# Optimization experiments

Measured on AMD Instinct MI355X. Metric: run time of the kernel, lower is better.

Reference implementation:

```python
import jax, jax.numpy as jnp
import numpy as np
import math

EPS = 1e-07
ITERATIONS = 3
FINAL_LAMBDA = 0.01

B, H, W, K, CIN, COUT, P = 8, 12, 12, 3, 16, 32, 16


def setup_inputs() -> dict:
    key = jax.random.key(0)
    k1, k2, k3, k4 = jax.random.split(key, 4)
    V = jax.random.normal(k1, (B, H, W, K, K, CIN, COUT, P), dtype=jnp.float32)
    a = jax.random.uniform(k2, (B, H, W, K, K, CIN, 1), dtype=jnp.float32)
    Beta_u = jax.random.normal(k3, (1, 1, 1, 1, 1, 1, COUT, 1), dtype=jnp.float32)
    Beta_a = jax.random.normal(k4, (1, 1, 1, 1, 1, 1, COUT), dtype=jnp.float32)
    R = jnp.full((B, H, W, K, K, CIN, COUT), 1.0 / COUT, dtype=jnp.float32)
    outSize = (B, H, W, COUT, P)
    return {"V": V, "a": a, "Beta_u": Beta_u, "Beta_a": Beta_a, "R": R, "outSize": outSize}


def _l2_normalize(x, axis):
    n = jnp.sqrt(jnp.sum(x * x, axis=axis, keepdims=True))
    return x / jnp.maximum(n, 1e-12)  # matches F.normalize default eps


def reference(V, a, Beta_u, Beta_a, R, outSize):
    mathpilog = jnp.log(jnp.asarray(2.0 * math.pi, dtype=jnp.float32))
    mu = sigma_sqr = a_out = None
    for i in range(ITERATIONS):
        Lam = FINAL_LAMBDA * (1.0 - 0.95 ** (i + 1))
        Rw = (R * a)[..., None]                                  # [B,h,w,K,K,Cin,Cout,1]
        mu_denom = jnp.sum(Rw, axis=(3, 4, 5), keepdims=True)    # [B,h,w,1,1,1,Cout,1]
        mu = jnp.sum(Rw * V, axis=(3, 4, 5), keepdims=True) / (mu_denom + EPS)  # [B,h,w,1,1,1,Cout,P]
        V_mu_sqr = (V - mu) ** 2                                 # [B,h,w,K,K,Cin,Cout,P]
        sigma_sqr = jnp.sum(Rw * V_mu_sqr, axis=(3, 4, 5), keepdims=True) / (mu_denom + EPS)
        cost_h = (Beta_u + 0.5 * jnp.log(sigma_sqr)) * mu_denom  # [B,h,w,1,1,1,Cout,P]
        x = Lam * (Beta_a - jnp.sum(cost_h, axis=7))             # [B,h,w,1,1,1,Cout]
        a_out = jax.nn.sigmoid(_l2_normalize(x, axis=6))
        log_p1 = -0.5 * jnp.sum(mathpilog + jnp.log(sigma_sqr), axis=7) + EPS
        log_p2 = -jnp.sum(V_mu_sqr / (2.0 * sigma_sqr + EPS), axis=7)  # [B,h,w,K,K,Cin,Cout]
        R = jax.nn.softmax(jnp.log(a_out) + log_p1 + log_p2, axis=6)
    mu_out = jnp.squeeze(mu).reshape(outSize)
    sigma_out = jnp.squeeze(sigma_sqr).reshape(outSize)
    return mu_out, jnp.squeeze(a_out), sigma_out
```

## Files before the change

### kernel.cpp

```cpp
#include <hip/hip_runtime.h>
#include <math.h>

#define NPOS 1152
#define NN   144
#define COUTC 32
#define PP   16
#define EPSF 1e-7f
#define LOG2PI 1.8378770664093453f

#define MU_OFF   0
#define A_OFF    589824
#define SIG_OFF  626688

typedef __attribute__((ext_vector_type(2))) __fp16    half2v;
typedef __attribute__((ext_vector_type(4))) float     f32x4;
typedef __attribute__((ext_vector_type(4))) unsigned  u32x4;

static __device__ __forceinline__ unsigned pk2(float a, float b) {
    half2v h = __builtin_amdgcn_cvt_pkrtz(a, b);
    return __builtin_bit_cast(unsigned, h);
}
static __device__ __forceinline__ void unpk2(unsigned u, float& a, float& b) {
    half2v h = __builtin_bit_cast(half2v, u);
    a = (float)h.x; b = (float)h.y;
}

template<int USE_HALF>
__global__ void __launch_bounds__(256)
em_routing_kernel(const float* __restrict__ V,
                  const float* __restrict__ a,
                  const float* __restrict__ Bu,
                  const float* __restrict__ Ba,
                  const float* __restrict__ Rin,
                  float* __restrict__ out,
                  u32x4* __restrict__ Vh)
{
    const int pos  = blockIdx.x;
    const int tid  = threadIdx.x;
    const int c    = tid & 31;
    const int slot = tid >> 5;
    const int wave = tid >> 6;

    const float* Vp = V + (size_t)pos * (NN * COUTC * PP);
    const float* Rp = Rin + (size_t)pos * (NN * COUTC);

    __shared__ float a_s[NN];
    __shared__ float red[4][COUTC][33];
    __shared__ float fin[COUTC][33];
    __shared__ float mu_s[COUTC][17];
    __shared__ float wp_s[COUTC][17];
    __shared__ float sg_s[COUTC][17];
    __shared__ float cl_s[COUTC];
    __shared__ float ao_s[COUTC];

    for (int i = tid; i < NN; i += 256) a_s[i] = a[pos * NN + i];
    __syncthreads();

    const float lam_tab[3] = {0.01f * (1.f - 0.95f),
                              0.01f * (1.f - 0.95f * 0.95f),
                              0.01f * (1.f - 0.95f * 0.95f * 0.95f)};

    auto reduce_finalize = [&](int it, float S0, float (&S1)[PP], float (&S2)[PP]) {
        S0 += __shfl_xor(S0, 32, 64);
        #pragma unroll
        for (int p = 0; p < PP; ++p) {
            S1[p] += __shfl_xor(S1[p], 32, 64);
            S2[p] += __shfl_xor(S2[p], 32, 64);
        }
        if ((tid & 32) == 0) {
            red[wave][c][0] = S0;
            #pragma unroll
            for (int p = 0; p < PP; ++p) {
                red[wave][c][1 + p]  = S1[p];
                red[wave][c][17 + p] = S2[p];
            }
        }
        __syncthreads();
        for (int idx = tid; idx < COUTC * 33; idx += 256) {
            int cc = idx / 33, k = idx - cc * 33;
            fin[cc][k] = red[0][cc][k] + red[1][cc][k] + red[2][cc][k] + red[3][cc][k];
        }
        __syncthreads();
        if (tid < 64) {
            float xv = 0.f, sumlog = 0.f;
            if (tid < 32) {
                const int cc = tid;
                float d0  = fin[cc][0];
                float inv = 1.f / (d0 + EPSF);
                #pragma unroll
                for (int p = 0; p < PP; ++p) {
                    float s1 = fin[cc][1 + p];
                    float s2 = fin[cc][17 + p];
                    float mu = s1 * inv;
                    float sg = (s2 - 2.f * mu * s1 + mu * mu * d0) * inv;
                    sg = fmaxf(sg, 1e-30f);
                    mu_s[cc][p] = mu;
                    sg_s[cc][p] = sg;
                    wp_s[cc][p] = 1.f / (2.f * sg + EPSF);
                    sumlog += logf(sg);
                }
                xv = lam_tab[it] * (Ba[cc] - d0 * (16.f * Bu[cc] + 0.5f * sumlog));
            }
            float ss = xv * xv;
            #pragma unroll
            for (int m = 1; m <= 32; m <<= 1) ss += __shfl_xor(ss, m, 64);
            if (tid < 32) {
                float y  = xv / fmaxf(sqrtf(ss), 1e-12f);
                float ao = 1.f / (1.f + expf(-y));
                ao_s[tid] = ao;
                cl_s[tid] = logf(ao) - 0.5f * (16.f * LOG2PI + sumlog) + EPSF;
            }
        }
        __syncthreads();
    };

    {
        float S0 = 0.f, S1[PP], S2[PP];
        #pragma unroll
        for (int p = 0; p < PP; ++p) { S1[p] = 0.f; S2[p] = 0.f; }

        #pragma unroll 3
        for (int j = 0; j < 18; ++j) {
            const int n = slot + (j << 3);
            const f32x4* vp = (const f32x4*)(Vp + (size_t)n * (COUTC * PP) + c * PP);
            f32x4 q0 = __builtin_nontemporal_load(vp);
            f32x4 q1 = __builtin_nontemporal_load(vp + 1);
            f32x4 q2 = __builtin_nontemporal_load(vp + 2);
            f32x4 q3 = __builtin_nontemporal_load(vp + 3);
            float v[PP] = {q0.x,q0.y,q0.z,q0.w, q1.x,q1.y,q1.z,q1.w,
                           q2.x,q2.y,q2.z,q2.w, q3.x,q3.y,q3.z,q3.w};
            if (USE_HALF) {
                size_t hb = ((size_t)(pos * NN + n) << 6) + (c << 1);
                u32x4 u0, u1;
                u0.x = pk2(v[0],  v[1]);  u0.y = pk2(v[2],  v[3]);
                u0.z = pk2(v[4],  v[5]);  u0.w = pk2(v[6],  v[7]);
                u1.x = pk2(v[8],  v[9]);  u1.y = pk2(v[10], v[11]);
                u1.z = pk2(v[12], v[13]); u1.w = pk2(v[14], v[15]);
                Vh[hb] = u0; Vh[hb + 1] = u1;
            }
            float Rw = __builtin_nontemporal_load(Rp + n * COUTC + c) * a_s[n];
            S0 += Rw;
            #pragma unroll
            for (int p = 0; p < PP; ++p) {
                float t = Rw * v[p];
                S1[p] += t;
                S2[p] = fmaf(t, v[p], S2[p]);
            }
        }
        reduce_finalize(0, S0, S1, S2);
    }

    for (int it = 1; it < 3; ++it) {
        float mu_r[PP], wp_r[PP];
        #pragma unroll
        for (int p = 0; p < PP; ++p) { mu_r[p] = mu_s[c][p]; wp_r[p] = wp_s[c][p]; }
        float cl_r = cl_s[c];
        #pragma unroll
        for (int p = 0; p < PP; ++p) {
            asm volatile("" : "+v"(mu_r[p]), "+v"(wp_r[p]));
        }
        asm volatile("" : "+v"(cl_r));

        float S0 = 0.f, S1[PP], S2[PP];
        #pragma unroll
        for (int p = 0; p < PP; ++p) { S1[p] = 0.f; S2[p] = 0.f; }

        for (int j = 0; j < 18; ++j) {
            const int n = slot + (j << 3);
            float v[PP];
            if (USE_HALF) {
                size_t hb = ((size_t)(pos * NN + n) << 6) + (c << 1);
                u32x4 u0 = Vh[hb], u1 = Vh[hb + 1];
                unsigned uu[8] = {u0.x, u0.y, u0.z, u0.w, u1.x, u1.y, u1.z, u1.w};
                #pragma unroll
                for (int k = 0; k < 8; ++k) unpk2(uu[k], v[2 * k], v[2 * k + 1]);
            } else {
                const f32x4* vp = (const f32x4*)(Vp + (size_t)n * (COUTC * PP) + c * PP);
                f32x4 q0 = vp[0], q1 = vp[1], q2 = vp[2], q3 = vp[3];
                v[0]=q0.x; v[1]=q0.y; v[2]=q0.z; v[3]=q0.w;
                v[4]=q1.x; v[5]=q1.y; v[6]=q1.z; v[7]=q1.w;
                v[8]=q2.x; v[9]=q2.y; v[10]=q2.z; v[11]=q2.w;
                v[12]=q3.x; v[13]=q3.y; v[14]=q3.z; v[15]=q3.w;
            }
            float acc = 0.f;
            #pragma unroll
            for (int p = 0; p < PP; ++p) {
                float d = v[p] - mu_r[p];
                acc = fmaf(d * wp_r[p], d, acc);
            }
            float logit = cl_r - acc;
            float m = logit;
            #pragma unroll
            for (int msk = 1; msk <= 16; msk <<= 1)
                m = fmaxf(m, __shfl_xor(m, msk, 64));
            float e = __expf(logit - m);
            float sum = e;
            #pragma unroll
            for (int msk = 1; msk <= 16; msk <<= 1)
                sum += __shfl_xor(sum, msk, 64);
            float Rw = (e / sum) * a_s[n];
            S0 += Rw;
            #pragma unroll
            for (int p = 0; p < PP; ++p) {
                float t = Rw * v[p];
                S1[p] += t;
                S2[p] = fmaf(t, v[p], S2[p]);
            }
        }
        reduce_finalize(it, S0, S1, S2);
    }

    for (int idx = tid; idx < COUTC * PP; idx += 256) {
        int cc = idx >> 4, p = idx & 15;
        out[MU_OFF  + (size_t)pos * (COUTC * PP) + idx] = mu_s[cc][p];
        out[SIG_OFF + (size_t)pos * (COUTC * PP) + idx] = sg_s[cc][p];
    }
    if (tid < COUTC) out[A_OFF + pos * COUTC + tid] = ao_s[tid];
}

extern "C" void kernel_launch(void* const* d_in, const int* in_sizes, int n_in,
                              void* d_out, int out_size, void* d_ws, size_t ws_size,
                              hipStream_t stream) {
    const float* V  = (const float*)d_in[0];
    const float* a  = (const float*)d_in[1];
    const float* Bu = (const float*)d_in[2];
    const float* Ba = (const float*)d_in[3];
    const float* R  = (const float*)d_in[4];
    float* out = (float*)d_out;
    const size_t need = (size_t)NPOS * NN * COUTC * PP * 2;
    if (ws_size >= need) {
        em_routing_kernel<1><<<NPOS, 256, 0, stream>>>(V, a, Bu, Ba, R, out, (u32x4*)d_ws);
    } else {
        em_routing_kernel<0><<<NPOS, 256, 0, stream>>>(V, a, Bu, Ba, R, out, (u32x4*)d_ws);
    }
}
```

Before: 578.6 us.

## Vectorize EM routing math to packed float2 and software-pipeline half loads

```diff
diff --git a/kernel.cpp b/kernel.cpp
--- a/kernel.cpp
+++ b/kernel.cpp
@@ -13,6 +13,7 @@
 #define SIG_OFF  626688
 
 typedef __attribute__((ext_vector_type(2))) __fp16    half2v;
+typedef __attribute__((ext_vector_type(2))) float     f32x2;
 typedef __attribute__((ext_vector_type(4))) float     f32x4;
 typedef __attribute__((ext_vector_type(4))) unsigned  u32x4;
 
@@ -20,20 +21,22 @@
     half2v h = __builtin_amdgcn_cvt_pkrtz(a, b);
     return __builtin_bit_cast(unsigned, h);
 }
-static __device__ __forceinline__ void unpk2(unsigned u, float& a, float& b) {
+static __device__ __forceinline__ f32x2 upk(unsigned u) {
     half2v h = __builtin_bit_cast(half2v, u);
-    a = (float)h.x; b = (float)h.y;
+    f32x2 r; r.x = (float)h.x; r.y = (float)h.y;
+    return r;
 }
 
 template<int USE_HALF>
-__global__ void __launch_bounds__(256)
+__global__ void __launch_bounds__(256, 4)
 em_routing_kernel(const float* __restrict__ V,
                   const float* __restrict__ a,
                   const float* __restrict__ Bu,
                   const float* __restrict__ Ba,
                   const float* __restrict__ Rin,
                   float* __restrict__ out,
-                  u32x4* __restrict__ Vh)
+                  const u32x4* __restrict__ VhR,
+                  u32x4* __restrict__ VhW)
 {
     const int pos  = blockIdx.x;
     const int tid  = threadIdx.x;
@@ -46,7 +49,6 @@
 
     __shared__ float a_s[NN];
     __shared__ float red[4][COUTC][33];
-    __shared__ float fin[COUTC][33];
     __shared__ float mu_s[COUTC][17];
     __shared__ float wp_s[COUTC][17];
     __shared__ float sg_s[COUTC][17];
@@ -60,64 +62,61 @@
                               0.01f * (1.f - 0.95f * 0.95f),
                               0.01f * (1.f - 0.95f * 0.95f * 0.95f)};
 
-    auto reduce_finalize = [&](int it, float S0, float (&S1)[PP], float (&S2)[PP]) {
+    auto reduce_finalize = [&](int it, float S0, f32x2 (&S1)[8], f32x2 (&S2)[8]) {
         S0 += __shfl_xor(S0, 32, 64);
         #pragma unroll
-        for (int p = 0; p < PP; ++p) {
-            S1[p] += __shfl_xor(S1[p], 32, 64);
-            S2[p] += __shfl_xor(S2[p], 32, 64);
+        for (int k = 0; k < 8; ++k) {
+            S1[k].x += __shfl_xor(S1[k].x, 32, 64);
+            S1[k].y += __shfl_xor(S1[k].y, 32, 64);
+            S2[k].x += __shfl_xor(S2[k].x, 32, 64);
+            S2[k].y += __shfl_xor(S2[k].y, 32, 64);
         }
         if ((tid & 32) == 0) {
             red[wave][c][0] = S0;
             #pragma unroll
+            for (int k = 0; k < 8; ++k) {
+                red[wave][c][1 + 2 * k]  = S1[k].x;
+                red[wave][c][2 + 2 * k]  = S1[k].y;
+                red[wave][c][17 + 2 * k] = S2[k].x;
+                red[wave][c][18 + 2 * k] = S2[k].y;
+            }
+        }
+        __syncthreads();
+        if (tid < 32) {
+            const int cc = tid;
+            float d0 = red[0][cc][0] + red[1][cc][0] + red[2][cc][0] + red[3][cc][0];
+            float inv = 1.f / (d0 + EPSF);
+            float sumlog = 0.f;
+            #pragma unroll
             for (int p = 0; p < PP; ++p) {
-                red[wave][c][1 + p]  = S1[p];
-                red[wave][c][17 + p] = S2[p];
-            }
-        }
-        __syncthreads();
-        for (int idx = tid; idx < COUTC * 33; idx += 256) {
-            int cc = idx / 33, k = idx - cc * 33;
-            fin[cc][k] = red[0][cc][k] + red[1][cc][k] + red[2][cc][k] + red[3][cc][k];
-        }
-        __syncthreads();
-        if (tid < 64) {
-            float xv = 0.f, sumlog = 0.f;
-            if (tid < 32) {
-                const int cc = tid;
-                float d0  = fin[cc][0];
-                float inv = 1.f / (d0 + EPSF);
-                #pragma unroll
-                for (int p = 0; p < PP; ++p) {
-                    float s1 = fin[cc][1 + p];
-                    float s2 = fin[cc][17 + p];
-                    float mu = s1 * inv;
-                    float sg = (s2 - 2.f * mu * s1 + mu * mu * d0) * inv;
-                    sg = fmaxf(sg, 1e-30f);
-                    mu_s[cc][p] = mu;
-                    sg_s[cc][p] = sg;
-                    wp_s[cc][p] = 1.f / (2.f * sg + EPSF);
-                    sumlog += logf(sg);
-                }
-                xv = lam_tab[it] * (Ba[cc] - d0 * (16.f * Bu[cc] + 0.5f * sumlog));
-            }
+                float s1 = red[0][cc][1 + p]  + red[1][cc][1 + p]
+                         + red[2][cc][1 + p]  + red[3][cc][1 + p];
+                float s2 = red[0][cc][17 + p] + red[1][cc][17 + p]
+                         + red[2][cc][17 + p] + red[3][cc][17 + p];
+                float mu = s1 * inv;
+                float sg = (s2 - 2.f * mu * s1 + mu * mu * d0) * inv;
+                sg = fmaxf(sg, 1e-30f);
+                mu_s[cc][p] = mu;
+                sg_s[cc][p] = sg;
+                wp_s[cc][p] = 1.f / (2.f * sg + EPSF);
+                sumlog += __logf(sg);
+            }
+            float xv = lam_tab[it] * (Ba[cc] - d0 * (16.f * Bu[cc] + 0.5f * sumlog));
             float ss = xv * xv;
             #pragma unroll
-            for (int m = 1; m <= 32; m <<= 1) ss += __shfl_xor(ss, m, 64);
-            if (tid < 32) {
-                float y  = xv / fmaxf(sqrtf(ss), 1e-12f);
-                float ao = 1.f / (1.f + expf(-y));
-                ao_s[tid] = ao;
-                cl_s[tid] = logf(ao) - 0.5f * (16.f * LOG2PI + sumlog) + EPSF;
-            }
+            for (int m = 1; m <= 16; m <<= 1) ss += __shfl_xor(ss, m, 64);
+            float y  = xv / fmaxf(sqrtf(ss), 1e-12f);
+            float ao = 1.f / (1.f + __expf(-y));
+            ao_s[cc] = ao;
+            cl_s[cc] = __logf(ao) - 0.5f * (16.f * LOG2PI + sumlog) + EPSF;
         }
         __syncthreads();
     };
 
     {
-        float S0 = 0.f, S1[PP], S2[PP];
-        #pragma unroll
-        for (int p = 0; p < PP; ++p) { S1[p] = 0.f; S2[p] = 0.f; }
+        float S0 = 0.f; f32x2 S1[8], S2[8];
+        #pragma unroll
+        for (int k = 0; k < 8; ++k) { S1[k] = (f32x2)0.f; S2[k] = (f32x2)0.f; }
 
         #pragma unroll 3
         for (int j = 0; j < 18; ++j) {
@@ -127,84 +126,123 @@
             f32x4 q1 = __builtin_nontemporal_load(vp + 1);
             f32x4 q2 = __builtin_nontemporal_load(vp + 2);
             f32x4 q3 = __builtin_nontemporal_load(vp + 3);
-            float v[PP] = {q0.x,q0.y,q0.z,q0.w, q1.x,q1.y,q1.z,q1.w,
-                           q2.x,q2.y,q2.z,q2.w, q3.x,q3.y,q3.z,q3.w};
+            f32x2 v2[8] = {{q0.x,q0.y},{q0.z,q0.w},{q1.x,q1.y},{q1.z,q1.w},
+                           {q2.x,q2.y},{q2.z,q2.w},{q3.x,q3.y},{q3.z,q3.w}};
             if (USE_HALF) {
                 size_t hb = ((size_t)(pos * NN + n) << 6) + (c << 1);
                 u32x4 u0, u1;
-                u0.x = pk2(v[0],  v[1]);  u0.y = pk2(v[2],  v[3]);
-                u0.z = pk2(v[4],  v[5]);  u0.w = pk2(v[6],  v[7]);
-                u1.x = pk2(v[8],  v[9]);  u1.y = pk2(v[10], v[11]);
-                u1.z = pk2(v[12], v[13]); u1.w = pk2(v[14], v[15]);
-                Vh[hb] = u0; Vh[hb + 1] = u1;
+                u0.x = pk2(v2[0].x, v2[0].y); u0.y = pk2(v2[1].x, v2[1].y);
+                u0.z = pk2(v2[2].x, v2[2].y); u0.w = pk2(v2[3].x, v2[3].y);
+                u1.x = pk2(v2[4].x, v2[4].y); u1.y = pk2(v2[5].x, v2[5].y);
+                u1.z = pk2(v2[6].x, v2[6].y); u1.w = pk2(v2[7].x, v2[7].y);
+                VhW[hb] = u0; VhW[hb + 1] = u1;
             }
             float Rw = __builtin_nontemporal_load(Rp + n * COUTC + c) * a_s[n];
             S0 += Rw;
-            #pragma unroll
-            for (int p = 0; p < PP; ++p) {
-                float t = Rw * v[p];
-                S1[p] += t;
-                S2[p] = fmaf(t, v[p], S2[p]);
+            f32x2 R2 = {Rw, Rw};
+            #pragma unroll
+            for (int k = 0; k < 8; ++k) {
+                f32x2 w = v2[k] * v2[k];
+                S1[k] += R2 * v2[k];
+                S2[k] += R2 * w;
             }
         }
         reduce_finalize(0, S0, S1, S2);
     }
 
     for (int it = 1; it < 3; ++it) {
-        float mu_r[PP], wp_r[PP];
-        #pragma unroll
-        for (int p = 0; p < PP; ++p) { mu_r[p] = mu_s[c][p]; wp_r[p] = wp_s[c][p]; }
+        f32x2 mu2[8], wp2[8];
+        #pragma unroll
+        for (int k = 0; k < 8; ++k) {
+            mu2[k].x = mu_s[c][2 * k];     mu2[k].y = mu_s[c][2 * k + 1];
+            wp2[k].x = wp_s[c][2 * k];     wp2[k].y = wp_s[c][2 * k + 1];
+        }
         float cl_r = cl_s[c];
-        #pragma unroll
-        for (int p = 0; p < PP; ++p) {
-            asm volatile("" : "+v"(mu_r[p]), "+v"(wp_r[p]));
-        }
-        asm volatile("" : "+v"(cl_r));
-
-        float S0 = 0.f, S1[PP], S2[PP];
-        #pragma unroll
-        for (int p = 0; p < PP; ++p) { S1[p] = 0.f; S2[p] = 0.f; }
-
-        for (int j = 0; j < 18; ++j) {
-            const int n = slot + (j << 3);
-            float v[PP];
-            if (USE_HALF) {
-                size_t hb = ((size_t)(pos * NN + n) << 6) + (c << 1);
-                u32x4 u0 = Vh[hb], u1 = Vh[hb + 1];
-                unsigned uu[8] = {u0.x, u0.y, u0.z, u0.w, u1.x, u1.y, u1.z, u1.w};
-                #pragma unroll
-                for (int k = 0; k < 8; ++k) unpk2(uu[k], v[2 * k], v[2 * k + 1]);
-            } else {
+
+        float S0 = 0.f; f32x2 S1[8], S2[8];
+        #pragma unroll
+        for (int k = 0; k < 8; ++k) { S1[k] = (f32x2)0.f; S2[k] = (f32x2)0.f; }
+
+        if (USE_HALF) {
+            const size_t base = ((size_t)(pos * NN + slot) << 6) + (c << 1);
+            u32x4 A0 = VhR[base],       A1 = VhR[base + 1];
+            u32x4 B0 = VhR[base + 512], B1 = VhR[base + 513];
+            for (int jj = 0; jj < 9; ++jj) {
+                size_t nb = base + (size_t)((jj < 8) ? (2 * jj + 2) : 0) * 512;
+                u32x4 C0 = VhR[nb],       C1 = VhR[nb + 1];
+                u32x4 D0 = VhR[nb + 512], D1 = VhR[nb + 513];
+                const int n0 = slot + (jj << 4), n1 = n0 + 8;
+
+                unsigned ua[8] = {A0.x,A0.y,A0.z,A0.w,A1.x,A1.y,A1.z,A1.w};
+                unsigned ub[8] = {B0.x,B0.y,B0.z,B0.w,B1.x,B1.y,B1.z,B1.w};
+                f32x2 va[8], vb[8];
+                #pragma unroll
+                for (int k = 0; k < 8; ++k) { va[k] = upk(ua[k]); vb[k] = upk(ub[k]); }
+
+                f32x2 acc0 = (f32x2)0.f, acc1 = (f32x2)0.f;
+                #pragma unroll
+                for (int k = 0; k < 8; ++k) {
+                    f32x2 d0 = va[k] - mu2[k]; acc0 += (d0 * d0) * wp2[k];
+                    f32x2 d1 = vb[k] - mu2[k]; acc1 += (d1 * d1) * wp2[k];
+                }
+                float l0 = cl_r - (acc0.x + acc0.y);
+                float l1 = cl_r - (acc1.x + acc1.y);
+                float m0 = l0, m1 = l1;
+                #pragma unroll
+                for (int msk = 1; msk <= 16; msk <<= 1) {
+                    m0 = fmaxf(m0, __shfl_xor(m0, msk, 64));
+                    m1 = fmaxf(m1, __shfl_xor(m1, msk, 64));
+                }
+                float e0 = __expf(l0 - m0), e1 = __expf(l1 - m1);
+                float s0 = e0, s1 = e1;
+                #pragma unroll
+                for (int msk = 1; msk <= 16; msk <<= 1) {
+                    s0 += __shfl_xor(s0, msk, 64);
+                    s1 += __shfl_xor(s1, msk, 64);
+                }
+                float Rw0 = (e0 / s0) * a_s[n0];
+                float Rw1 = (e1 / s1) * a_s[n1];
+                S0 += Rw0 + Rw1;
+                f32x2 R0 = {Rw0, Rw0}, R1 = {Rw1, Rw1};
+                #pragma unroll
+                for (int k = 0; k < 8; ++k) {
+                    S1[k] += R0 * va[k];
+                    S2[k] += R0 * (va[k] * va[k]);
+                    S1[k] += R1 * vb[k];
+                    S2[k] += R1 * (vb[k] * vb[k]);
+                }
+                A0 = C0; A1 = C1; B0 = D0; B1 = D1;
+            }
+        } else {
+            for (int j = 0; j < 18; ++j) {
+                const int n = slot + (j << 3);
                 const f32x4* vp = (const f32x4*)(Vp + (size_t)n * (COUTC * PP) + c * PP);
                 f32x4 q0 = vp[0], q1 = vp[1], q2 = vp[2], q3 = vp[3];
-                v[0]=q0.x; v[1]=q0.y; v[2]=q0.z; v[3]=q0.w;
-                v[4]=q1.x; v[5]=q1.y; v[6]=q1.z; v[7]=q1.w;
-                v[8]=q2.x; v[9]=q2.y; v[10]=q2.z; v[11]=q2.w;
-                v[12]=q3.x; v[13]=q3.y; v[14]=q3.z; v[15]=q3.w;
-            }
-            float acc = 0.f;
-            #pragma unroll
-            for (int p = 0; p < PP; ++p) {
-                float d = v[p] - mu_r[p];
-                acc = fmaf(d * wp_r[p], d, acc);
-            }
-            float logit = cl_r - acc;
-            float m = logit;
-            #pragma unroll
-            for (int msk = 1; msk <= 16; msk <<= 1)
-                m = fmaxf(m, __shfl_xor(m, msk, 64));
-            float e = __expf(logit - m);
-            float sum = e;
-            #pragma unroll
-            for (int msk = 1; msk <= 16; msk <<= 1)
-                sum += __shfl_xor(sum, msk, 64);
-            float Rw = (e / sum) * a_s[n];
-            S0 += Rw;
-            #pragma unroll
-            for (int p = 0; p < PP; ++p) {
-                float t = Rw * v[p];
-                S1[p] += t;
-                S2[p] = fmaf(t, v[p], S2[p]);
+                f32x2 va[8] = {{q0.x,q0.y},{q0.z,q0.w},{q1.x,q1.y},{q1.z,q1.w},
+                               {q2.x,q2.y},{q2.z,q2.w},{q3.x,q3.y},{q3.z,q3.w}};
+                f32x2 acc = (f32x2)0.f;
+                #pragma unroll
+                for (int k = 0; k < 8; ++k) {
+                    f32x2 d = va[k] - mu2[k]; acc += (d * d) * wp2[k];
+                }
+                float logit = cl_r - (acc.x + acc.y);
+                float m = logit;
+                #pragma unroll
+                for (int msk = 1; msk <= 16; msk <<= 1)
+                    m = fmaxf(m, __shfl_xor(m, msk, 64));
+                float e = __expf(logit - m);
+                float sum = e;
+                #pragma unroll
+                for (int msk = 1; msk <= 16; msk <<= 1)
+                    sum += __shfl_xor(sum, msk, 64);
+                float Rw = (e / sum) * a_s[n];
+                S0 += Rw;
+                f32x2 R2 = {Rw, Rw};
+                #pragma unroll
+                for (int k = 0; k < 8; ++k) {
+                    S1[k] += R2 * va[k];
+                    S2[k] += R2 * (va[k] * va[k]);
+                }
             }
         }
         reduce_finalize(it, S0, S1, S2);
@@ -229,8 +267,10 @@
     float* out = (float*)d_out;
     const size_t need = (size_t)NPOS * NN * COUTC * PP * 2;
     if (ws_size >= need) {
-        em_routing_kernel<1><<<NPOS, 256, 0, stream>>>(V, a, Bu, Ba, R, out, (u32x4*)d_ws);
+        em_routing_kernel<1><<<NPOS, 256, 0, stream>>>(V, a, Bu, Ba, R, out,
+                                                       (const u32x4*)d_ws, (u32x4*)d_ws);
     } else {
-        em_routing_kernel<0><<<NPOS, 256, 0, stream>>>(V, a, Bu, Ba, R, out, (u32x4*)d_ws);
-    }
-}
+        em_routing_kernel<0><<<NPOS, 256, 0, stream>>>(V, a, Bu, Ba, R, out,
+                                                       (const u32x4*)d_ws, (u32x4*)d_ws);
+    }
+}
```

After: 595.9 us. 1.03x slower.
